# Kernel optimization log

Hardware: AMD Instinct MI355X
Metric: run time of the kernel (lower is better)

The kernel has to match this reference:

```python
import jax, jax.numpy as jnp
import numpy as np

N = 100000
E = 1600000
D_IN = 128
D_OUT = 128
NEG_SLOPE = 0.01  # PyTorch LeakyReLU default


def setup_inputs() -> dict:
    key = jax.random.key(0)
    ks = jax.random.split(key, 6)
    x = jax.random.normal(ks[0], (N, D_IN), dtype=jnp.float32)
    src = jax.random.randint(ks[1], (E,), 0, N, dtype=jnp.int32)
    dst = jax.random.randint(ks[2], (E,), 0, N, dtype=jnp.int32)
    e_attn = jax.random.uniform(ks[3], (E,), dtype=jnp.float32)
    # Xavier-normal-ish init for linear weights
    std = float(np.sqrt(2.0 / (D_IN + D_OUT)))
    W1 = jax.random.normal(ks[4], (D_OUT, D_IN), dtype=jnp.float32) * std
    W2 = jax.random.normal(ks[5], (D_OUT, D_IN), dtype=jnp.float32) * std
    b1 = jnp.zeros((D_OUT,), dtype=jnp.float32)
    b2 = jnp.zeros((D_OUT,), dtype=jnp.float32)
    return {"x": x, "src": src, "dst": dst, "e_attn": e_attn,
            "W1": W1, "b1": b1, "W2": W2, "b2": b2}


def leaky_relu(v):
    return jnp.where(v >= 0, v, NEG_SLOPE * v)


def reference(x, src, dst, e_attn, W1, b1, W2, b2):
    # Edge-weighted gather-scatter: h_n[d] = sum_{e: dst(e)=d} a_e * x[src(e)]
    msgs = x[src] * e_attn[:, None]                      # [E, D_IN]
    h_n = jax.ops.segment_sum(msgs, dst, num_segments=N)  # [N, D_IN]
    # Bi-interaction: LeakyReLU(W1(x + h_n)) + LeakyReLU(W2(x * h_n))
    add_part = leaky_relu(jnp.einsum('nd,od->no', x + h_n, W1) + b1)
    mul_part = leaky_relu(jnp.einsum('nd,od->no', x * h_n, W2) + b2)
    return add_part + mul_part  # dropout p=0.0 -> identity
```

## Files before the change

### kernel.cpp

```cpp
#include <hip/hip_runtime.h>

#define N_NODES 100000
#define E_EDGES 1600000
#define D 128
#define AP 132
#define ASTR 136

typedef short s16x8 __attribute__((ext_vector_type(8)));
typedef float f32x4 __attribute__((ext_vector_type(4)));

__device__ __forceinline__ unsigned short f2bf(float f) {
    union { float f; unsigned u; } v;
    v.f = f;
    unsigned r = v.u + 0x7FFFu + ((v.u >> 16) & 1u);
    return (unsigned short)(r >> 16);
}

__device__ __forceinline__ float bf2f(unsigned short u) {
    union { unsigned u; float f; } v;
    v.u = ((unsigned)u) << 16;
    return v.f;
}

__device__ __forceinline__ float lrelu(float v) {
    return v >= 0.0f ? v : 0.01f * v;
}

__global__ __launch_bounds__(256) void xconv_kernel(
    const float* __restrict__ x, unsigned short* __restrict__ xbf) {
    int idx = blockIdx.x * 256 + threadIdx.x;
    const float4* xp = (const float4*)(x) + (size_t)idx * 2;
    float4 a = xp[0], b = xp[1];
    ushort4 lo, hi;
    lo.x = f2bf(a.x); lo.y = f2bf(a.y); lo.z = f2bf(a.z); lo.w = f2bf(a.w);
    hi.x = f2bf(b.x); hi.y = f2bf(b.y); hi.z = f2bf(b.z); hi.w = f2bf(b.w);
    ushort4* dp = (ushort4*)(xbf) + (size_t)idx * 2;
    dp[0] = lo; dp[1] = hi;
}


__global__ __launch_bounds__(256) void hist_kernel(
    const int* __restrict__ dst, int* __restrict__ cnt,
    int* __restrict__ rank, int E) {
    int e = blockIdx.x * 256 + threadIdx.x;
    if (e < E) rank[e] = atomicAdd(&cnt[dst[e]], 1);
}

__global__ __launch_bounds__(256) void scanA_kernel(
    const int* __restrict__ cnt, int* __restrict__ excl,
    int* __restrict__ bsum, int n) {
    __shared__ int tmp[256];
    int gid = blockIdx.x * 256 + threadIdx.x;
    int v = (gid < n) ? cnt[gid] : 0;
    tmp[threadIdx.x] = v;
    __syncthreads();
    for (int ofs = 1; ofs < 256; ofs <<= 1) {
        int t = (threadIdx.x >= ofs) ? tmp[threadIdx.x - ofs] : 0;
        __syncthreads();
        tmp[threadIdx.x] += t;
        __syncthreads();
    }
    int incl = tmp[threadIdx.x];
    if (gid < n) excl[gid] = incl - v;
    if (threadIdx.x == 255) bsum[blockIdx.x] = incl;
}

__global__ __launch_bounds__(512) void scanB_kernel(int* __restrict__ bsum, int nb) {
    __shared__ int tmp[512];
    int v = (threadIdx.x < nb) ? bsum[threadIdx.x] : 0;
    tmp[threadIdx.x] = v;
    __syncthreads();
    for (int ofs = 1; ofs < 512; ofs <<= 1) {
        int t = (threadIdx.x >= ofs) ? tmp[threadIdx.x - ofs] : 0;
        __syncthreads();
        tmp[threadIdx.x] += t;
        __syncthreads();
    }
    if (threadIdx.x < nb) bsum[threadIdx.x] = tmp[threadIdx.x] - v;
}

__global__ __launch_bounds__(256) void scanC_kernel(
    const int* __restrict__ excl, const int* __restrict__ bsumExcl,
    int* __restrict__ off, int n, int E) {
    int gid = blockIdx.x * 256 + threadIdx.x;
    if (gid < n) off[gid] = excl[gid] + bsumExcl[gid >> 8];
    if (gid == 0) off[n] = E;
}

__global__ __launch_bounds__(256) void fill_kernel(
    const int* __restrict__ src, const int* __restrict__ dst,
    const float* __restrict__ ea, const int* __restrict__ off,
    const int* __restrict__ rank, int2* __restrict__ csr, int E) {
    int e = blockIdx.x * 256 + threadIdx.x;
    if (e >= E) return;
    int d = dst[e];
    int pos = off[d] + rank[e];
    csr[pos] = make_int2(src[e], __float_as_int(ea[e]));
}

__global__ __launch_bounds__(256) void gather_bf_kernel(
    const unsigned short* __restrict__ xbf, const int2* __restrict__ csr,
    const int* __restrict__ off, float* __restrict__ h) {
    int node = blockIdx.x * 4 + (threadIdx.x >> 6);
    int lane = threadIdx.x & 63;
    int half = lane >> 5;
    int li = lane & 31;
    int beg = off[node];
    int nE = off[node + 1] - beg;

    float4 acc0 = make_float4(0.f, 0.f, 0.f, 0.f);
    float4 acc1 = make_float4(0.f, 0.f, 0.f, 0.f);
    int i = half;
    for (; i + 2 < nE; i += 4) {
        int2 p0 = csr[beg + i];
        int2 p1 = csr[beg + i + 2];
        float a0 = __int_as_float(p0.y);
        float a1 = __int_as_float(p1.y);
        ushort4 v0 = ((const ushort4*)(xbf + (size_t)p0.x * D))[li];
        ushort4 v1 = ((const ushort4*)(xbf + (size_t)p1.x * D))[li];
        acc0.x += a0 * bf2f(v0.x); acc0.y += a0 * bf2f(v0.y);
        acc0.z += a0 * bf2f(v0.z); acc0.w += a0 * bf2f(v0.w);
        acc1.x += a1 * bf2f(v1.x); acc1.y += a1 * bf2f(v1.y);
        acc1.z += a1 * bf2f(v1.z); acc1.w += a1 * bf2f(v1.w);
    }
    if (i < nE) {
        int2 p0 = csr[beg + i];
        float a0 = __int_as_float(p0.y);
        ushort4 v0 = ((const ushort4*)(xbf + (size_t)p0.x * D))[li];
        acc0.x += a0 * bf2f(v0.x); acc0.y += a0 * bf2f(v0.y);
        acc0.z += a0 * bf2f(v0.z); acc0.w += a0 * bf2f(v0.w);
    }
    acc0.x += acc1.x; acc0.y += acc1.y; acc0.z += acc1.z; acc0.w += acc1.w;
    float4 oth;
    oth.x = __shfl(acc0.x, lane ^ 32);
    oth.y = __shfl(acc0.y, lane ^ 32);
    oth.z = __shfl(acc0.z, lane ^ 32);
    oth.w = __shfl(acc0.w, lane ^ 32);
    acc0.x += oth.x; acc0.y += oth.y; acc0.z += oth.z; acc0.w += oth.w;
    if (half == 0)
        ((float4*)(h + (size_t)node * D))[li] = acc0;
}

__global__ __launch_bounds__(256) void gather_f32_kernel(
    const float* __restrict__ x, const int2* __restrict__ csr,
    const int* __restrict__ off, float* __restrict__ h) {
    int node = blockIdx.x * 4 + (threadIdx.x >> 6);
    int lane = threadIdx.x & 63;
    int beg = off[node];
    int end = off[node + 1];
    float2 acc0 = make_float2(0.f, 0.f);
    float2 acc1 = make_float2(0.f, 0.f);
    int e = beg;
    for (; e + 1 < end; e += 2) {
        int2 p0 = csr[e];
        int2 p1 = csr[e + 1];
        float a0 = __int_as_float(p0.y);
        float a1 = __int_as_float(p1.y);
        float2 v0 = ((const float2*)(x + (size_t)p0.x * D))[lane];
        float2 v1 = ((const float2*)(x + (size_t)p1.x * D))[lane];
        acc0.x += a0 * v0.x; acc0.y += a0 * v0.y;
        acc1.x += a1 * v1.x; acc1.y += a1 * v1.y;
    }
    if (e < end) {
        int2 p0 = csr[e];
        float a0 = __int_as_float(p0.y);
        float2 v0 = ((const float2*)(x + (size_t)p0.x * D))[lane];
        acc0.x += a0 * v0.x; acc0.y += a0 * v0.y;
    }
    acc0.x += acc1.x; acc0.y += acc1.y;
    ((float2*)(h + (size_t)node * D))[lane] = acc0;
}

__global__ __launch_bounds__(256) void scatter_kernel(
    const float* __restrict__ x, const int* __restrict__ src,
    const int* __restrict__ dst, const float* __restrict__ ea,
    float* __restrict__ h, int E) {
    int idx = blockIdx.x * 256 + threadIdx.x;
    int e = idx >> 5;
    int lane = idx & 31;
    if (e >= E) return;
    int s = src[e];
    int d = dst[e];
    float a = ea[e];
    float4 v = ((const float4*)(x + (size_t)s * D))[lane];
    float* hp = h + (size_t)d * D + lane * 4;
    atomicAdd(hp + 0, a * v.x);
    atomicAdd(hp + 1, a * v.y);
    atomicAdd(hp + 2, a * v.z);
    atomicAdd(hp + 3, a * v.w);
}

__global__ __launch_bounds__(256) void wconv_kernel(
    const float* __restrict__ W1, const float* __restrict__ W2,
    unsigned short* __restrict__ Wswz) {
    int tid = blockIdx.x * 256 + threadIdx.x;
    if (tid >= 2 * 4 * 8 * 64) return;
    int lane = tid & 63;
    int ct   = (tid >> 6) & 7;
    int ks   = (tid >> 9) & 3;
    int mat  = tid >> 11;
    const float* W = mat ? W2 : W1;
    int o  = ct * 16 + (lane & 15);
    int k0 = ks * 32 + (lane >> 4) * 8;
    const float* sp = W + (size_t)o * D + k0;
    unsigned short* dp = Wswz + (size_t)tid * 8;
    ushort4 lo, hi;
    lo.x = f2bf(sp[0]); lo.y = f2bf(sp[1]); lo.z = f2bf(sp[2]); lo.w = f2bf(sp[3]);
    hi.x = f2bf(sp[4]); hi.y = f2bf(sp[5]); hi.z = f2bf(sp[6]); hi.w = f2bf(sp[7]);
    *(ushort4*)(dp + 0) = lo;
    *(ushort4*)(dp + 4) = hi;
}

template <bool XBF>
__global__ __launch_bounds__(256, 4) void mfma_gemm_kernel(
    const float* __restrict__ xf, const unsigned short* __restrict__ xb,
    const float* __restrict__ h, const unsigned short* __restrict__ Wswz,
    const float* __restrict__ b1, const float* __restrict__ b2,
    float* __restrict__ out) {
    __shared__ unsigned short A[2][64 * ASTR];

    const int n0 = blockIdx.x * 64;
    const int t = threadIdx.x;
    const int lane = t & 63;
    const int wv = t >> 6;

#pragma unroll
    for (int i = 0; i < 8; ++i) {
        int s = t + i * 256;
        int row = s >> 5;
        int c4 = s & 31;
        int srcrow = n0 + row;
        if (srcrow >= N_NODES) srcrow = N_NODES - 1;
        float4 xv;
        if (XBF) {
            ushort4 xu = ((const ushort4*)(xb + (size_t)srcrow * D))[c4];
            xv = make_float4(bf2f(xu.x), bf2f(xu.y), bf2f(xu.z), bf2f(xu.w));
        } else {
            xv = ((const float4*)(xf + (size_t)srcrow * D))[c4];
        }
        float4 hv = ((const float4*)(h + (size_t)srcrow * D))[c4];
        ushort4 av, mv;
        av.x = f2bf(xv.x + hv.x); av.y = f2bf(xv.y + hv.y);
        av.z = f2bf(xv.z + hv.z); av.w = f2bf(xv.w + hv.w);
        mv.x = f2bf(xv.x * hv.x); mv.y = f2bf(xv.y * hv.y);
        mv.z = f2bf(xv.z * hv.z); mv.w = f2bf(xv.w * hv.w);
        *(ushort4*)&A[0][row * ASTR + c4 * 4] = av;
        *(ushort4*)&A[1][row * ASTR + c4 * 4] = mv;
    }

    s16x8 Bf[2][2][4];
    float bb1[2], bb2[2];
#pragma unroll
    for (int ci = 0; ci < 2; ++ci) {
        int ct = wv + ci * 4;
        bb1[ci] = b1[ct * 16 + (lane & 15)];
        bb2[ci] = b2[ct * 16 + (lane & 15)];
#pragma unroll
        for (int mat = 0; mat < 2; ++mat)
#pragma unroll
            for (int ks = 0; ks < 4; ++ks)
                Bf[ci][mat][ks] = *(const s16x8*)(
                    Wswz + ((size_t)(((mat * 4 + ks) * 8 + ct) * 64 + lane)) * 8);
    }

    __syncthreads();

    const int quad = lane >> 4;
    const int kq = quad * 8;

#pragma unroll
    for (int mt = 0; mt < 4; ++mt) {
        f32x4 acc[2][2];
#pragma unroll
        for (int ci = 0; ci < 2; ++ci)
#pragma unroll
            for (int p = 0; p < 2; ++p) acc[ci][p] = (f32x4){0.f, 0.f, 0.f, 0.f};

        const int arow = mt * 16 + (lane & 15);
#pragma unroll
        for (int ks = 0; ks < 4; ++ks) {
            s16x8 a0 = *(const s16x8*)&A[0][arow * ASTR + ks * 32 + kq];
            s16x8 a1 = *(const s16x8*)&A[1][arow * ASTR + ks * 32 + kq];
#pragma unroll
            for (int ci = 0; ci < 2; ++ci) {
                acc[ci][0] = __builtin_amdgcn_mfma_f32_16x16x32_bf16(
                    a0, Bf[ci][0][ks], acc[ci][0], 0, 0, 0);
                acc[ci][1] = __builtin_amdgcn_mfma_f32_16x16x32_bf16(
                    a1, Bf[ci][1][ks], acc[ci][1], 0, 0, 0);
            }
        }

#pragma unroll
        for (int ci = 0; ci < 2; ++ci) {
            int oc = (wv + ci * 4) * 16 + (lane & 15);
#pragma unroll
            for (int r = 0; r < 4; ++r) {
                int node = n0 + mt * 16 + quad * 4 + r;
                if (node < N_NODES) {
                    float v = lrelu(acc[ci][0][r] + bb1[ci])
                            + lrelu(acc[ci][1][r] + bb2[ci]);
                    out[(size_t)node * D + oc] = v;
                }
            }
        }
    }
}

__global__ __launch_bounds__(256) void gemm_kernel(
    const float* __restrict__ x, const float* __restrict__ h,
    const float* __restrict__ W1, const float* __restrict__ b1,
    const float* __restrict__ W2, const float* __restrict__ b2,
    float* __restrict__ out) {
    __shared__ float Aadd[32 * AP];
    __shared__ float Amul[32 * AP];
    const int n0 = blockIdx.x * 32;
    const int t = threadIdx.x;
#pragma unroll
    for (int i = 0; i < 4; ++i) {
        int fi = t + i * 256;
        int row = fi >> 5;
        int c4 = fi & 31;
        float4 xv = ((const float4*)(x + (size_t)(n0 + row) * D))[c4];
        float4 hv = ((const float4*)(h + (size_t)(n0 + row) * D))[c4];
        float4 av = make_float4(xv.x + hv.x, xv.y + hv.y, xv.z + hv.z, xv.w + hv.w);
        float4 mv = make_float4(xv.x * hv.x, xv.y * hv.y, xv.z * hv.z, xv.w * hv.w);
        *((float4*)&Aadd[row * AP + c4 * 4]) = av;
        *((float4*)&Amul[row * AP + c4 * 4]) = mv;
    }
    __syncthreads();
    const int m0 = (t >> 5) * 4;
    const int o0 = (t & 31) * 4;
    float acc1[4][4];
    float acc2[4][4];
#pragma unroll
    for (int i = 0; i < 4; ++i)
#pragma unroll
        for (int j = 0; j < 4; ++j) { acc1[i][j] = 0.0f; acc2[i][j] = 0.0f; }
#pragma unroll 4
    for (int d = 0; d < D; d += 4) {
        float4 a[4], m[4], w1[4], w2[4];
#pragma unroll
        for (int i = 0; i < 4; ++i) a[i] = *(const float4*)&Aadd[(m0 + i) * AP + d];
#pragma unroll
        for (int i = 0; i < 4; ++i) m[i] = *(const float4*)&Amul[(m0 + i) * AP + d];
#pragma unroll
        for (int j = 0; j < 4; ++j) w1[j] = *(const float4*)&W1[(size_t)(o0 + j) * D + d];
#pragma unroll
        for (int j = 0; j < 4; ++j) w2[j] = *(const float4*)&W2[(size_t)(o0 + j) * D + d];
#pragma unroll
        for (int i = 0; i < 4; ++i)
#pragma unroll
            for (int j = 0; j < 4; ++j) {
                acc1[i][j] += a[i].x * w1[j].x + a[i].y * w1[j].y
                            + a[i].z * w1[j].z + a[i].w * w1[j].w;
                acc2[i][j] += m[i].x * w2[j].x + m[i].y * w2[j].y
                            + m[i].z * w2[j].z + m[i].w * w2[j].w;
            }
    }
#pragma unroll
    for (int i = 0; i < 4; ++i) {
        float4 r;
        float v1, v2;
        v1 = lrelu(acc1[i][0] + b1[o0 + 0]); v2 = lrelu(acc2[i][0] + b2[o0 + 0]); r.x = v1 + v2;
        v1 = lrelu(acc1[i][1] + b1[o0 + 1]); v2 = lrelu(acc2[i][1] + b2[o0 + 1]); r.y = v1 + v2;
        v1 = lrelu(acc1[i][2] + b1[o0 + 2]); v2 = lrelu(acc2[i][2] + b2[o0 + 2]); r.z = v1 + v2;
        v1 = lrelu(acc1[i][3] + b1[o0 + 3]); v2 = lrelu(acc2[i][3] + b2[o0 + 3]); r.w = v1 + v2;
        ((float4*)(out + (size_t)(n0 + m0 + i) * D))[t & 31] = r;
    }
}

extern "C" void kernel_launch(void* const* d_in, const int* in_sizes, int n_in,
                              void* d_out, int out_size, void* d_ws, size_t ws_size,
                              hipStream_t stream) {
    const float* x   = (const float*)d_in[0];
    const int*   src = (const int*)d_in[1];
    const int*   dst = (const int*)d_in[2];
    const float* ea  = (const float*)d_in[3];
    const float* W1  = (const float*)d_in[4];
    const float* b1  = (const float*)d_in[5];
    const float* W2  = (const float*)d_in[6];
    const float* b2  = (const float*)d_in[7];
    float* out = (float*)d_out;

    float* h = out;

    const size_t SZ_WSWZ = 2 * 4 * 8 * 64 * 8 * sizeof(unsigned short);
    const size_t SZ_CNT  = (size_t)N_NODES * sizeof(int);
    const size_t SZ_OFF  = (size_t)(N_NODES + 1) * sizeof(int);
    const size_t SZ_BSUM = 512 * sizeof(int);
    const size_t SZ_RANK = (size_t)E_EDGES * sizeof(int);
    const size_t SZ_CSR  = (size_t)E_EDGES * sizeof(int2);
    const size_t SZ_XBF  = (size_t)N_NODES * D * sizeof(unsigned short);
    auto align256 = [](size_t v) { return (v + 255) & ~(size_t)255; };
    size_t o_wswz = 0;
    size_t o_cnt  = o_wswz + align256(SZ_WSWZ);
    size_t o_off  = o_cnt + align256(SZ_CNT);
    size_t o_excl = o_off + align256(SZ_OFF);
    size_t o_bsum = o_excl + align256(SZ_CNT);
    size_t o_rank = o_bsum + align256(SZ_BSUM);
    size_t o_csr  = o_rank + align256(SZ_RANK);
    size_t o_xbf  = o_csr + align256(SZ_CSR);
    size_t need_t1 = o_xbf;
    size_t need_t2 = o_xbf + align256(SZ_XBF);

    const int NB_E = (E_EDGES + 255) / 256;
    const int NB_N = (N_NODES + 255) / 256;

    char* ws = (char*)d_ws;
    unsigned short* Wswz = (unsigned short*)(ws + o_wswz);
    int*   cnt  = (int*)(ws + o_cnt);
    int*   off  = (int*)(ws + o_off);
    int*   excl = (int*)(ws + o_excl);
    int*   bsum = (int*)(ws + o_bsum);
    int*   rank = (int*)(ws + o_rank);
    int2*  csr  = (int2*)(ws + o_csr);
    unsigned short* xbf = (unsigned short*)(ws + o_xbf);

    bool t2 = ws_size >= need_t2;
    bool t1 = ws_size >= need_t1;

    if (t1 || t2) {
        hipMemsetAsync(cnt, 0, SZ_CNT, stream);
        if (t2) xconv_kernel<<<(N_NODES * D / 8 + 255) / 256, 256, 0, stream>>>(x, xbf);
        hist_kernel<<<NB_E, 256, 0, stream>>>(dst, cnt, rank, E_EDGES);
        scanA_kernel<<<NB_N, 256, 0, stream>>>(cnt, excl, bsum, N_NODES);
        scanB_kernel<<<1, 512, 0, stream>>>(bsum, NB_N);
        scanC_kernel<<<NB_N, 256, 0, stream>>>(excl, bsum, off, N_NODES, E_EDGES);
        fill_kernel<<<NB_E, 256, 0, stream>>>(src, dst, ea, off, rank, csr, E_EDGES);
        if (t2)
            gather_bf_kernel<<<N_NODES / 4, 256, 0, stream>>>(xbf, csr, off, h);
        else
            gather_f32_kernel<<<N_NODES / 4, 256, 0, stream>>>(x, csr, off, h);

        wconv_kernel<<<16, 256, 0, stream>>>(W1, W2, Wswz);
        int blocks = (N_NODES + 63) / 64;
        if (t2)
            mfma_gemm_kernel<true><<<blocks, 256, 0, stream>>>(x, xbf, h, Wswz, b1, b2, out);
        else
            mfma_gemm_kernel<false><<<blocks, 256, 0, stream>>>(x, xbf, h, Wswz, b1, b2, out);
    } else {
        hipMemsetAsync(h, 0, (size_t)N_NODES * D * sizeof(float), stream);
        int total = E_EDGES * 32;
        scatter_kernel<<<(total + 255) / 256, 256, 0, stream>>>(x, src, dst, ea,
                                                                h, E_EDGES);
        gemm_kernel<<<N_NODES / 32, 256, 0, stream>>>(x, h, W1, b1, W2, b2, out);
    }
}
```

Before: 331.8 us.

## Fuse CSR gather into MFMA GEMM and compact histogram rank storage

The gather of neighbour features is folded into the GEMM kernel: each block gathers its 64 nodes' aggregated features, builds the bf16 x+h and x*h tiles directly in shared memory, and keeps the weights in registers for the MFMA. This removes the fp32 h round-trip through global memory. The histogram counters are padded to a 16-int stride to reduce atomic contention, the rank array shrinks to bytes, and the separate excl buffer is dropped. The byte-sized rank assumes no node has more than 255 incoming edges, and the fused kernel runs with less parallelism during the gather phase, since each wave walks 16 nodes in turn.

```diff
diff --git a/kernel.cpp b/kernel.cpp
--- a/kernel.cpp
+++ b/kernel.cpp
@@ -38,20 +38,19 @@
     dp[0] = lo; dp[1] = hi;
 }
 
-
 __global__ __launch_bounds__(256) void hist_kernel(
     const int* __restrict__ dst, int* __restrict__ cnt,
-    int* __restrict__ rank, int E) {
+    unsigned char* __restrict__ rank, int E, int stride) {
     int e = blockIdx.x * 256 + threadIdx.x;
-    if (e < E) rank[e] = atomicAdd(&cnt[dst[e]], 1);
+    if (e < E) rank[e] = (unsigned char)atomicAdd(&cnt[(size_t)dst[e] * stride], 1);
 }
 
 __global__ __launch_bounds__(256) void scanA_kernel(
-    const int* __restrict__ cnt, int* __restrict__ excl,
-    int* __restrict__ bsum, int n) {
+    const int* __restrict__ cnt, int* __restrict__ off,
+    int* __restrict__ bsum, int n, int stride) {
     __shared__ int tmp[256];
     int gid = blockIdx.x * 256 + threadIdx.x;
-    int v = (gid < n) ? cnt[gid] : 0;
+    int v = (gid < n) ? cnt[(size_t)gid * stride] : 0;
     tmp[threadIdx.x] = v;
     __syncthreads();
     for (int ofs = 1; ofs < 256; ofs <<= 1) {
@@ -61,7 +60,7 @@
         __syncthreads();
     }
     int incl = tmp[threadIdx.x];
-    if (gid < n) excl[gid] = incl - v;
+    if (gid < n) off[gid] = incl - v;
     if (threadIdx.x == 255) bsum[blockIdx.x] = incl;
 }
 
@@ -80,65 +79,149 @@
 }
 
 __global__ __launch_bounds__(256) void scanC_kernel(
-    const int* __restrict__ excl, const int* __restrict__ bsumExcl,
-    int* __restrict__ off, int n, int E) {
+    const int* __restrict__ bsumExcl, int* __restrict__ off, int n, int E) {
     int gid = blockIdx.x * 256 + threadIdx.x;
-    if (gid < n) off[gid] = excl[gid] + bsumExcl[gid >> 8];
+    if (gid < n) off[gid] += bsumExcl[gid >> 8];
     if (gid == 0) off[n] = E;
 }
 
 __global__ __launch_bounds__(256) void fill_kernel(
     const int* __restrict__ src, const int* __restrict__ dst,
     const float* __restrict__ ea, const int* __restrict__ off,
-    const int* __restrict__ rank, int2* __restrict__ csr, int E) {
+    const unsigned char* __restrict__ rank, int2* __restrict__ csr, int E) {
     int e = blockIdx.x * 256 + threadIdx.x;
     if (e >= E) return;
     int d = dst[e];
-    int pos = off[d] + rank[e];
+    int pos = off[d] + (int)rank[e];
     csr[pos] = make_int2(src[e], __float_as_int(ea[e]));
 }
 
-__global__ __launch_bounds__(256) void gather_bf_kernel(
+__global__ __launch_bounds__(256, 4) void fused_gemm_kernel(
     const unsigned short* __restrict__ xbf, const int2* __restrict__ csr,
-    const int* __restrict__ off, float* __restrict__ h) {
-    int node = blockIdx.x * 4 + (threadIdx.x >> 6);
-    int lane = threadIdx.x & 63;
-    int half = lane >> 5;
-    int li = lane & 31;
-    int beg = off[node];
-    int nE = off[node + 1] - beg;
-
-    float4 acc0 = make_float4(0.f, 0.f, 0.f, 0.f);
-    float4 acc1 = make_float4(0.f, 0.f, 0.f, 0.f);
-    int i = half;
-    for (; i + 2 < nE; i += 4) {
-        int2 p0 = csr[beg + i];
-        int2 p1 = csr[beg + i + 2];
-        float a0 = __int_as_float(p0.y);
-        float a1 = __int_as_float(p1.y);
-        ushort4 v0 = ((const ushort4*)(xbf + (size_t)p0.x * D))[li];
-        ushort4 v1 = ((const ushort4*)(xbf + (size_t)p1.x * D))[li];
-        acc0.x += a0 * bf2f(v0.x); acc0.y += a0 * bf2f(v0.y);
-        acc0.z += a0 * bf2f(v0.z); acc0.w += a0 * bf2f(v0.w);
-        acc1.x += a1 * bf2f(v1.x); acc1.y += a1 * bf2f(v1.y);
-        acc1.z += a1 * bf2f(v1.z); acc1.w += a1 * bf2f(v1.w);
-    }
-    if (i < nE) {
-        int2 p0 = csr[beg + i];
-        float a0 = __int_as_float(p0.y);
-        ushort4 v0 = ((const ushort4*)(xbf + (size_t)p0.x * D))[li];
-        acc0.x += a0 * bf2f(v0.x); acc0.y += a0 * bf2f(v0.y);
-        acc0.z += a0 * bf2f(v0.z); acc0.w += a0 * bf2f(v0.w);
-    }
-    acc0.x += acc1.x; acc0.y += acc1.y; acc0.z += acc1.z; acc0.w += acc1.w;
-    float4 oth;
-    oth.x = __shfl(acc0.x, lane ^ 32);
-    oth.y = __shfl(acc0.y, lane ^ 32);
-    oth.z = __shfl(acc0.z, lane ^ 32);
-    oth.w = __shfl(acc0.w, lane ^ 32);
-    acc0.x += oth.x; acc0.y += oth.y; acc0.z += oth.z; acc0.w += oth.w;
-    if (half == 0)
-        ((float4*)(h + (size_t)node * D))[li] = acc0;
+    const int* __restrict__ off, const unsigned short* __restrict__ Wswz,
+    const float* __restrict__ b1, const float* __restrict__ b2,
+    float* __restrict__ out) {
+    __shared__ unsigned short A[2][64 * ASTR];
+
+    const int n0 = blockIdx.x * 64;
+    const int t = threadIdx.x;
+    const int lane = t & 63;
+    const int wv = t >> 6;
+    const int half = lane >> 5;
+    const int li = lane & 31;
+
+    s16x8 Bf[2][2][4];
+    float bb1[2], bb2[2];
+#pragma unroll
+    for (int ci = 0; ci < 2; ++ci) {
+        int ct = wv + ci * 4;
+        bb1[ci] = b1[ct * 16 + (lane & 15)];
+        bb2[ci] = b2[ct * 16 + (lane & 15)];
+#pragma unroll
+        for (int mat = 0; mat < 2; ++mat)
+#pragma unroll
+            for (int ks = 0; ks < 4; ++ks)
+                Bf[ci][mat][ks] = *(const s16x8*)(
+                    Wswz + ((size_t)(((mat * 4 + ks) * 8 + ct) * 64 + lane)) * 8);
+    }
+
+    for (int j = 0; j < 16; ++j) {
+        int row = wv * 16 + j;
+        int node = n0 + row;
+        float4 hacc = make_float4(0.f, 0.f, 0.f, 0.f);
+        if (node < N_NODES) {
+            int beg = off[node];
+            int end = off[node + 1];
+            float4 acc1 = make_float4(0.f, 0.f, 0.f, 0.f);
+            int i = beg + half;
+            for (; i + 2 < end; i += 4) {
+                int2 p0 = csr[i];
+                int2 p1 = csr[i + 2];
+                float a0 = __int_as_float(p0.y);
+                float a1 = __int_as_float(p1.y);
+                ushort4 v0 = ((const ushort4*)(xbf + (size_t)p0.x * D))[li];
+                ushort4 v1 = ((const ushort4*)(xbf + (size_t)p1.x * D))[li];
+                hacc.x += a0 * bf2f(v0.x); hacc.y += a0 * bf2f(v0.y);
+                hacc.z += a0 * bf2f(v0.z); hacc.w += a0 * bf2f(v0.w);
+                acc1.x += a1 * bf2f(v1.x); acc1.y += a1 * bf2f(v1.y);
+                acc1.z += a1 * bf2f(v1.z); acc1.w += a1 * bf2f(v1.w);
+            }
+            if (i < end) {
+                int2 p0 = csr[i];
+                float a0 = __int_as_float(p0.y);
+                ushort4 v0 = ((const ushort4*)(xbf + (size_t)p0.x * D))[li];
+                hacc.x += a0 * bf2f(v0.x); hacc.y += a0 * bf2f(v0.y);
+                hacc.z += a0 * bf2f(v0.z); hacc.w += a0 * bf2f(v0.w);
+            }
+            hacc.x += acc1.x; hacc.y += acc1.y;
+            hacc.z += acc1.z; hacc.w += acc1.w;
+        }
+        float4 oth;
+        oth.x = __shfl(hacc.x, lane ^ 32);
+        oth.y = __shfl(hacc.y, lane ^ 32);
+        oth.z = __shfl(hacc.z, lane ^ 32);
+        oth.w = __shfl(hacc.w, lane ^ 32);
+        hacc.x += oth.x; hacc.y += oth.y; hacc.z += oth.z; hacc.w += oth.w;
+
+        if (half == 0) {
+            ushort4 av, mv;
+            if (node < N_NODES) {
+                ushort4 xu = ((const ushort4*)(xbf + (size_t)node * D))[li];
+                float4 xv = make_float4(bf2f(xu.x), bf2f(xu.y), bf2f(xu.z), bf2f(xu.w));
+                av.x = f2bf(xv.x + hacc.x); av.y = f2bf(xv.y + hacc.y);
+                av.z = f2bf(xv.z + hacc.z); av.w = f2bf(xv.w + hacc.w);
+                mv.x = f2bf(xv.x * hacc.x); mv.y = f2bf(xv.y * hacc.y);
+                mv.z = f2bf(xv.z * hacc.z); mv.w = f2bf(xv.w * hacc.w);
+            } else {
+                av = make_ushort4(0, 0, 0, 0);
+                mv = make_ushort4(0, 0, 0, 0);
+            }
+            *(ushort4*)&A[0][row * ASTR + li * 4] = av;
+            *(ushort4*)&A[1][row * ASTR + li * 4] = mv;
+        }
+    }
+
+    __syncthreads();
+
+    const int quad = lane >> 4;
+    const int kq = quad * 8;
+
+#pragma unroll
+    for (int mt = 0; mt < 4; ++mt) {
+        f32x4 acc[2][2];
+#pragma unroll
+        for (int ci = 0; ci < 2; ++ci)
+#pragma unroll
+            for (int p = 0; p < 2; ++p) acc[ci][p] = (f32x4){0.f, 0.f, 0.f, 0.f};
+
+        const int arow = mt * 16 + (lane & 15);
+#pragma unroll
+        for (int ks = 0; ks < 4; ++ks) {
+            s16x8 a0 = *(const s16x8*)&A[0][arow * ASTR + ks * 32 + kq];
+            s16x8 a1 = *(const s16x8*)&A[1][arow * ASTR + ks * 32 + kq];
+#pragma unroll
+            for (int ci = 0; ci < 2; ++ci) {
+                acc[ci][0] = __builtin_amdgcn_mfma_f32_16x16x32_bf16(
+                    a0, Bf[ci][0][ks], acc[ci][0], 0, 0, 0);
+                acc[ci][1] = __builtin_amdgcn_mfma_f32_16x16x32_bf16(
+                    a1, Bf[ci][1][ks], acc[ci][1], 0, 0, 0);
+            }
+        }
+
+#pragma unroll
+        for (int ci = 0; ci < 2; ++ci) {
+            int oc = (wv + ci * 4) * 16 + (lane & 15);
+#pragma unroll
+            for (int r = 0; r < 4; ++r) {
+                int node = n0 + mt * 16 + quad * 4 + r;
+                if (node < N_NODES) {
+                    float v = lrelu(acc[ci][0][r] + bb1[ci])
+                            + lrelu(acc[ci][1][r] + bb2[ci]);
+                    out[(size_t)node * D + oc] = v;
+                }
+            }
+        }
+    }
 }
 
 __global__ __launch_bounds__(256) void gather_f32_kernel(
@@ -211,10 +294,9 @@
     *(ushort4*)(dp + 4) = hi;
 }
 
-template <bool XBF>
 __global__ __launch_bounds__(256, 4) void mfma_gemm_kernel(
-    const float* __restrict__ xf, const unsigned short* __restrict__ xb,
-    const float* __restrict__ h, const unsigned short* __restrict__ Wswz,
+    const float* __restrict__ xf, const float* __restrict__ h,
+    const unsigned short* __restrict__ Wswz,
     const float* __restrict__ b1, const float* __restrict__ b2,
     float* __restrict__ out) {
     __shared__ unsigned short A[2][64 * ASTR];
@@ -231,13 +313,7 @@
         int c4 = s & 31;
         int srcrow = n0 + row;
         if (srcrow >= N_NODES) srcrow = N_NODES - 1;
-        float4 xv;
-        if (XBF) {
-            ushort4 xu = ((const ushort4*)(xb + (size_t)srcrow * D))[c4];
-            xv = make_float4(bf2f(xu.x), bf2f(xu.y), bf2f(xu.z), bf2f(xu.w));
-        } else {
-            xv = ((const float4*)(xf + (size_t)srcrow * D))[c4];
-        }
+        float4 xv = ((const float4*)(xf + (size_t)srcrow * D))[c4];
         float4 hv = ((const float4*)(h + (size_t)srcrow * D))[c4];
         ushort4 av, mv;
         av.x = f2bf(xv.x + hv.x); av.y = f2bf(xv.y + hv.y);
@@ -382,63 +458,75 @@
     const float* b2  = (const float*)d_in[7];
     float* out = (float*)d_out;
 
-    float* h = out;
+    auto align256 = [](size_t v) { return (v + 255) & ~(size_t)255; };
 
     const size_t SZ_WSWZ = 2 * 4 * 8 * 64 * 8 * sizeof(unsigned short);
-    const size_t SZ_CNT  = (size_t)N_NODES * sizeof(int);
     const size_t SZ_OFF  = (size_t)(N_NODES + 1) * sizeof(int);
     const size_t SZ_BSUM = 512 * sizeof(int);
-    const size_t SZ_RANK = (size_t)E_EDGES * sizeof(int);
+    const size_t SZ_RANK = (size_t)E_EDGES;
     const size_t SZ_CSR  = (size_t)E_EDGES * sizeof(int2);
     const size_t SZ_XBF  = (size_t)N_NODES * D * sizeof(unsigned short);
-    auto align256 = [](size_t v) { return (v + 255) & ~(size_t)255; };
-    size_t o_wswz = 0;
-    size_t o_cnt  = o_wswz + align256(SZ_WSWZ);
-    size_t o_off  = o_cnt + align256(SZ_CNT);
-    size_t o_excl = o_off + align256(SZ_OFF);
-    size_t o_bsum = o_excl + align256(SZ_CNT);
-    size_t o_rank = o_bsum + align256(SZ_BSUM);
-    size_t o_csr  = o_rank + align256(SZ_RANK);
-    size_t o_xbf  = o_csr + align256(SZ_CSR);
-    size_t need_t1 = o_xbf;
-    size_t need_t2 = o_xbf + align256(SZ_XBF);
+
+    struct Lay { size_t o_wswz, o_cnt, o_off, o_bsum, o_rank, o_csr, o_xbf,
+                 need_fused, need_t1, sz_cnt; };
+    auto mk = [&](int stride) {
+        Lay L;
+        L.sz_cnt = (size_t)N_NODES * stride * sizeof(int);
+        L.o_wswz = 0;
+        L.o_cnt  = L.o_wswz + align256(SZ_WSWZ);
+        L.o_off  = L.o_cnt + align256(L.sz_cnt);
+        L.o_bsum = L.o_off + align256(SZ_OFF);
+        L.o_rank = L.o_bsum + align256(SZ_BSUM);
+        L.o_csr  = L.o_rank + align256(SZ_RANK);
+        L.o_xbf  = L.o_csr + align256(SZ_CSR);
+        L.need_t1 = L.o_xbf;
+        L.need_fused = L.o_xbf + align256(SZ_XBF);
+        return L;
+    };
+
+    Lay L16 = mk(16), L1 = mk(1);
+    int stride;
+    Lay L;
+    bool fused_ok, t1_ok;
+    if (ws_size >= L16.need_fused)      { stride = 16; L = L16; fused_ok = true;  t1_ok = true; }
+    else if (ws_size >= L1.need_fused)  { stride = 1;  L = L1;  fused_ok = true;  t1_ok = true; }
+    else if (ws_size >= L1.need_t1)     { stride = 1;  L = L1;  fused_ok = false; t1_ok = true; }
+    else                                { stride = 1;  L = L1;  fused_ok = false; t1_ok = false; }
 
     const int NB_E = (E_EDGES + 255) / 256;
     const int NB_N = (N_NODES + 255) / 256;
 
     char* ws = (char*)d_ws;
-    unsigned short* Wswz = (unsigned short*)(ws + o_wswz);
-    int*   cnt  = (int*)(ws + o_cnt);
-    int*   off  = (int*)(ws + o_off);
-    int*   excl = (int*)(ws + o_excl);
-    int*   bsum = (int*)(ws + o_bsum);
-    int*   rank = (int*)(ws + o_rank);
-    int2*  csr  = (int2*)(ws + o_csr);
-    unsigned short* xbf = (unsigned short*)(ws + o_xbf);
-
-    bool t2 = ws_size >= need_t2;
-    bool t1 = ws_size >= need_t1;
-
-    if (t1 || t2) {
-        hipMemsetAsync(cnt, 0, SZ_CNT, stream);
-        if (t2) xconv_kernel<<<(N_NODES * D / 8 + 255) / 256, 256, 0, stream>>>(x, xbf);
-        hist_kernel<<<NB_E, 256, 0, stream>>>(dst, cnt, rank, E_EDGES);
-        scanA_kernel<<<NB_N, 256, 0, stream>>>(cnt, excl, bsum, N_NODES);
+    unsigned short* Wswz = (unsigned short*)(ws + L.o_wswz);
+    int*   cnt  = (int*)(ws + L.o_cnt);
+    int*   off  = (int*)(ws + L.o_off);
+    int*   bsum = (int*)(ws + L.o_bsum);
+    unsigned char* rank = (unsigned char*)(ws + L.o_rank);
+    int2*  csr  = (int2*)(ws + L.o_csr);
+    unsigned short* xbf = (unsigned short*)(ws + L.o_xbf);
+
+    if (t1_ok) {
+        hipMemsetAsync(cnt, 0, L.sz_cnt, stream);
+        if (fused_ok)
+            xconv_kernel<<<(N_NODES * D / 8 + 255) / 256, 256, 0, stream>>>(x, xbf);
+        hist_kernel<<<NB_E, 256, 0, stream>>>(dst, cnt, rank, E_EDGES, stride);
+        scanA_kernel<<<NB_N, 256, 0, stream>>>(cnt, off, bsum, N_NODES, stride);
         scanB_kernel<<<1, 512, 0, stream>>>(bsum, NB_N);
-        scanC_kernel<<<NB_N, 256, 0, stream>>>(excl, bsum, off, N_NODES, E_EDGES);
+        scanC_kernel<<<NB_N, 256, 0, stream>>>(bsum, off, N_NODES, E_EDGES);
         fill_kernel<<<NB_E, 256, 0, stream>>>(src, dst, ea, off, rank, csr, E_EDGES);
-        if (t2)
-            gather_bf_kernel<<<N_NODES / 4, 256, 0, stream>>>(xbf, csr, off, h);
-        else
+        wconv_kernel<<<16, 256, 0, stream>>>(W1, W2, Wswz);
+
+        int blocks = (N_NODES + 63) / 64;
+        if (fused_ok) {
+            fused_gemm_kernel<<<blocks, 256, 0, stream>>>(xbf, csr, off, Wswz,
+                                                          b1, b2, out);
+        } else {
+            float* h = out;
             gather_f32_kernel<<<N_NODES / 4, 256, 0, stream>>>(x, csr, off, h);
-
-        wconv_kernel<<<16, 256, 0, stream>>>(W1, W2, Wswz);
-        int blocks = (N_NODES + 63) / 64;
-        if (t2)
-            mfma_gemm_kernel<true><<<blocks, 256, 0, stream>>>(x, xbf, h, Wswz, b1, b2, out);
-        else
-            mfma_gemm_kernel<false><<<blocks, 256, 0, stream>>>(x, xbf, h, Wswz, b1, b2, out);
+            mfma_gemm_kernel<<<blocks, 256, 0, stream>>>(x, h, Wswz, b1, b2, out);
+        }
     } else {
+        float* h = out;
         hipMemsetAsync(h, 0, (size_t)N_NODES * D * sizeof(float), stream);
         int total = E_EDGES * 32;
         scatter_kernel<<<(total + 255) / 256, 256, 0, stream>>>(x, src, dst, ea,
```

Result: slower. 377.1 us (+13.7%).
